# Kernel optimization log

Measured on AMD Instinct MI355X. Metric: run time of the kernel, lower is better.

Reference implementation:

```python
import jax, jax.numpy as jnp
import numpy as np

N_CAM = 6
N_HEADS = 8
N_POINTS = 4
D = 256  # internal d_model of the deformable attention


def _sine_pos(h, w, d=D):
    # DETR PositionEmbeddingSine, normalize=True, channels-last (h, w, d)
    npf = d // 2
    two_pi = 2.0 * np.pi
    y = jnp.arange(1, h + 1, dtype=jnp.float32) / (h + 1e-6) * two_pi
    x = jnp.arange(1, w + 1, dtype=jnp.float32) / (w + 1e-6) * two_pi
    dim_t = (10000.0 ** (2.0 * (jnp.arange(npf) // 2) / npf)).astype(jnp.float32)
    def enc(v):
        p = v[:, None] / dim_t
        return jnp.stack([jnp.sin(p[:, 0::2]), jnp.cos(p[:, 1::2])], axis=-1).reshape(v.shape[0], -1)
    py, px = enc(y), enc(x)
    return jnp.concatenate([
        jnp.broadcast_to(py[:, None, :], (h, w, npf)),
        jnp.broadcast_to(px[None, :, :], (h, w, npf))], axis=-1)


def _layernorm(x, g, b, eps=1e-5):
    mu = jnp.mean(x, -1, keepdims=True)
    var = jnp.mean((x - mu) ** 2, -1, keepdims=True)
    return (x - mu) * jax.lax.rsqrt(var + eps) * g + b


def _bilinear_gather(kv, loc_x, loc_y, H, W):
    # kv: (b, L, heads, H*W, c); loc_*: (b, Lq, heads, L, P) normalized to [0,1]
    # emulates F.grid_sample(mode='bilinear', padding_mode='zeros', align_corners=False)
    b, L, heads, HW, c = kv.shape
    _, Lq, _, _, P = loc_x.shape
    x = loc_x * W - 0.5
    y = loc_y * H - 0.5
    x0 = jnp.floor(x)
    y0 = jnp.floor(y)
    fx = x - x0
    fy = y - y0
    out = jnp.zeros((b, Lq, heads, L, P, c), kv.dtype)
    for dx in (0, 1):
        for dy in (0, 1):
            xi = x0 + dx
            yi = y0 + dy
            valid = (xi >= 0) & (xi < W) & (yi >= 0) & (yi < H)
            wgt = (fx if dx else 1.0 - fx) * (fy if dy else 1.0 - fy) * valid
            idx = (jnp.clip(yi, 0, H - 1) * W + jnp.clip(xi, 0, W - 1)).astype(jnp.int32)
            idx_t = idx.transpose(0, 3, 2, 1, 4).reshape(b, L, heads, Lq * P, 1)
            g = jnp.take_along_axis(kv, idx_t, axis=3)
            g = g.reshape(b, L, heads, Lq, P, c).transpose(0, 3, 2, 1, 4, 5)
            out = out + wgt[..., None] * g
    return out  # (b, Lq, heads, L, P, c)


def reference(x, conv0_w, conv0_b, conv2_w, conv2_b, cam_emb,
              off_w, off_b, val_w, val_b, key_w, key_b, out_w, out_b,
              conv1_w, conv1_b, norm0_g, norm0_b,
              lin1_w, lin1_b, lin2_w, lin2_b, norm2_g, norm2_b):
    bn, dim, H, W = x.shape
    b = bn // N_CAM
    hd = D // N_HEADS
    HW = H * W
    Lq = N_CAM * HW

    x_nhwc = x.transpose(0, 2, 3, 1)                  # (bn, H, W, dim)
    residual = x_nhwc.reshape(b, Lq, dim)             # b (n h w) d

    src = (x_nhwc @ conv0_w.T + conv0_b).reshape(b, N_CAM, H, W, D)  # conv0 1x1

    pos = _sine_pos(H, W)                              # (H, W, 256)
    spc = src + pos[None, None] + cam_emb[None, :, None, None, :]
    # per-level global descriptor: mean over pixels of conv2(src+pos+cam)
    g = jnp.mean((spc @ conv2_w.T + conv2_b).reshape(b, N_CAM, HW, D), axis=2)  # (b, n, 256)

    src_flat = src.reshape(b, Lq, D)
    query = spc.reshape(b, Lq, D)                      # src + cam + pos (flattened)

    value = src_flat @ val_w.T + val_b
    keys = src_flat @ key_w.T + key_b

    # sampling locations: per-query reference point + learned offsets (normalized)
    offsets = (query @ off_w.T + off_b).reshape(b, Lq, N_HEADS, N_CAM, N_POINTS, 2)
    ry, rx = jnp.meshgrid(
        (jnp.arange(H, dtype=jnp.float32) + 0.5) / H,
        (jnp.arange(W, dtype=jnp.float32) + 0.5) / W, indexing='ij')
    ref = jnp.tile(jnp.stack([rx.ravel(), ry.ravel()], -1), (N_CAM, 1))  # (Lq, 2) as (x, y)
    loc = ref[None, :, None, None, None, :] + offsets / jnp.array([W, H], jnp.float32)

    # gather keys and values in a single bilinear pass (concat on channel)
    kv = jnp.concatenate([
        keys.reshape(b, N_CAM, HW, N_HEADS, hd),
        value.reshape(b, N_CAM, HW, N_HEADS, hd)], axis=-1).transpose(0, 1, 3, 2, 4)
    sampled = _bilinear_gather(kv, loc[..., 0], loc[..., 1], H, W)  # (b,Lq,heads,L,P,2hd)
    k_s, v_s = sampled[..., :hd], sampled[..., hd:]

    # append per-level global token as an extra key/value point per level
    g_h = g.reshape(b, 1, N_CAM, N_HEADS, hd).transpose(0, 1, 3, 2, 4)[:, :, :, :, None, :]
    g_h = jnp.broadcast_to(g_h, (b, Lq, N_HEADS, N_CAM, 1, hd))
    k_all = jnp.concatenate([k_s, g_h], axis=4)        # (b,Lq,heads,L,P+1,hd)
    v_all = jnp.concatenate([v_s, g_h], axis=4)

    # key-aware attention: softmax over all (level, point) sampled keys
    q_h = query.reshape(b, Lq, N_HEADS, hd)
    logits = jnp.einsum('bqhd,bqhlpd->bqhlp', q_h, k_all) / jnp.sqrt(jnp.float32(hd))
    attn = jax.nn.softmax(logits.reshape(b, Lq, N_HEADS, -1), axis=-1).reshape(logits.shape)
    attn_out = jnp.einsum('bqhlp,bqhlpd->bqhd', attn, v_all).reshape(b, Lq, D)
    attn_out = attn_out @ out_w.T + out_b

    out = attn_out @ conv1_w.T + conv1_b               # conv1 1x1 back to dim
    out = _layernorm(residual + out, norm0_g, norm0_b)
    ffn = jax.nn.relu(out @ lin1_w.T + lin1_b) @ lin2_w.T + lin2_b
    out = _layernorm(out + ffn, norm2_g, norm2_b)

    return out.reshape(b, N_CAM, H, W, dim).transpose(0, 1, 4, 2, 3).reshape(bn, dim, H, W)


def setup_inputs() -> dict:
    key = jax.random.key(0)
    ks = jax.random.split(key, 16)
    B, DIM, H, W = 1, 256, 20, 40

    def w(k, shape, s=0.02):
        return jax.random.normal(k, shape, jnp.float32) * s

    n_off = N_HEADS * N_CAM * N_POINTS * 2
    return {
        "x": jax.random.normal(ks[0], (B * N_CAM, DIM, H, W), jnp.float32),
        "conv0_w": w(ks[1], (D, DIM)), "conv0_b": jnp.zeros((D,), jnp.float32),
        "conv2_w": w(ks[2], (D, D)), "conv2_b": jnp.zeros((D,), jnp.float32),
        "cam_emb": jax.random.uniform(ks[3], (N_CAM, D), jnp.float32),
        "off_w": w(ks[4], (n_off, D)),
        "off_b": jax.random.normal(ks[5], (n_off,), jnp.float32) * 0.5,
        "val_w": w(ks[6], (D, D)), "val_b": jnp.zeros((D,), jnp.float32),
        "key_w": w(ks[7], (D, D)), "key_b": jnp.zeros((D,), jnp.float32),
        "out_w": w(ks[8], (D, D)), "out_b": jnp.zeros((D,), jnp.float32),
        "conv1_w": w(ks[9], (DIM, D)), "conv1_b": jnp.zeros((DIM,), jnp.float32),
        "norm0_g": jnp.ones((DIM,), jnp.float32), "norm0_b": jnp.zeros((DIM,), jnp.float32),
        "lin1_w": w(ks[10], (DIM, DIM)), "lin1_b": jnp.zeros((DIM,), jnp.float32),
        "lin2_w": w(ks[11], (DIM, DIM)), "lin2_b": jnp.zeros((DIM,), jnp.float32),
        "norm2_g": jnp.ones((DIM,), jnp.float32), "norm2_b": jnp.zeros((DIM,), jnp.float32),
    }
```

## Files before the change

kernel.cpp:

```cpp
#include <hip/hip_runtime.h>
#include <math.h>

typedef unsigned short u16;
typedef unsigned int u32;

#define NCAM 6
#define NHEADS 8
#define NPOINTS 4
#define DD 256
#define HH 20
#define WW 40
#define HWSZ 800
#define LQ 4800
#define HDIM 32

typedef __attribute__((ext_vector_type(8))) short bf16x8;
typedef __attribute__((ext_vector_type(4))) float f32x4;

__device__ __forceinline__ u16 f2b(float x) {
    union { float f; u32 u; } v;
    v.f = x;
    u32 r = (v.u + 0x7FFFu + ((v.u >> 16) & 1u)) >> 16;
    return (u16)r;
}
__device__ __forceinline__ float lo2f(u32 u) {
    union { u32 u; float f; } v; v.u = u << 16; return v.f;
}
__device__ __forceinline__ float hi2f(u32 u) {
    union { u32 u; float f; } v; v.u = u & 0xFFFF0000u; return v.f;
}
__device__ __forceinline__ float red16(float s) {
    s += __shfl_xor(s, 1);
    s += __shfl_xor(s, 2);
    s += __shfl_xor(s, 4);
    s += __shfl_xor(s, 8);
    return s;
}

#define P1_BLOCKS 4570
__global__ __launch_bounds__(256) void prep1(
    const float* __restrict__ x, const float* __restrict__ conv0_w,
    const float* __restrict__ conv0_b, const float* __restrict__ key_w,
    const float* __restrict__ key_b, const float* __restrict__ val_w,
    const float* __restrict__ val_b, const float* __restrict__ off_w,
    const float* __restrict__ off_b, const float* __restrict__ lin1_w,
    const float* __restrict__ lin2_w, const float* __restrict__ conv1_w,
    const float* __restrict__ conv1_b, const float* __restrict__ out_w,
    const float* __restrict__ out_b, const float* __restrict__ cam_emb,
    float* __restrict__ pos, u16* __restrict__ xtb, float* __restrict__ mu_x,
    u16* __restrict__ Wcat, float* __restrict__ bias_cat,
    u16* __restrict__ conv1b, u16* __restrict__ lin1b, u16* __restrict__ lin2b,
    u16* __restrict__ off_wb, u16* __restrict__ kvpackb,
    u16* __restrict__ conv0_wTb, u16* __restrict__ out_wTb,
    float* __restrict__ bcomb, float* __restrict__ camoff,
    float* __restrict__ posy, float* __restrict__ posx) {
    __shared__ float sbuf[1088];
    int b = blockIdx.x, t = threadIdx.x;
    if (b < 800) {
        int hw = b, d = t;
        int h = hw / WW, w = hw % WW;
        int j = (d & 127) >> 1;
        float dim = powf(10000.0f, (float)j * (1.0f / 64.0f));
        float v;
        if (d < 128) v = (float)(h + 1) / (20.0f + 1e-6f) * (2.0f * (float)M_PI);
        else         v = (float)(w + 1) / (40.0f + 1e-6f) * (2.0f * (float)M_PI);
        float p = v / dim;
        pos[hw * DD + d] = (d & 1) ? cosf(p) : sinf(p);
    } else if (b < 1184) {
        int row = (b - 800) * 4 + (t >> 6);
        int lane = t & 63;
        const float* base = x + (size_t)row * HWSZ;
        float s = 0.f;
        for (int i = lane; i < HWSZ; i += 64) s += base[i];
#pragma unroll
        for (int m = 1; m <= 32; m <<= 1) s += __shfl_xor(s, m);
        if (lane == 0) mu_x[row] = s * (1.0f / (float)HWSZ);
    } else if (b < 3104) {
        int i = (b - 1184) * 256 + t;
        if (i < 65536) {
            Wcat[i] = f2b(conv0_w[i]);
            if (i < 256) bias_cat[i] = conv0_b[i];
        } else if (i < 131072) {
            conv1b[i - 65536] = f2b(conv1_w[i - 65536]);
        } else if (i < 196608) {
            lin1b[i - 131072] = f2b(lin1_w[i - 131072]);
        } else if (i < 262144) {
            lin2b[i - 196608] = f2b(lin2_w[i - 196608]);
        } else if (i < 360448) {
            off_wb[i - 262144] = f2b(off_w[i - 262144]);
        } else {
            int j = i - 360448;
            int rj = j >> 8, k = j & 255;
            int head = rj >> 6, cpair = (rj >> 1) & 31, kv = rj & 1;
            kvpackb[j] = f2b((kv ? val_w : key_w)[(size_t)(head * 32 + cpair) * 256 + k]);
        }
    } else if (b < 3232) {
        int idx = b - 3104;
        int which = idx >> 6;
        int t2 = idx & 63;
        int k0 = (t2 >> 3) * 32, c0 = (t2 & 7) * 32;
        const float* src = which ? out_w : conv0_w;
        u16* dst = which ? out_wTb : conv0_wTb;
        float (*tile)[33] = (float(*)[33])sbuf;
        int lc = t & 31, lk4 = t >> 5;
#pragma unroll
        for (int i = 0; i < 4; ++i) {
            int lk = lk4 * 4 + i;
            tile[lk][lc] = src[(size_t)(k0 + lk) * 256 + c0 + lc];
        }
        __syncthreads();
        int lk2 = t & 31, lc4 = t >> 5;
#pragma unroll
        for (int i = 0; i < 4; ++i) {
            int lc2 = lc4 * 4 + i;
            dst[(size_t)(c0 + lc2) * 256 + k0 + lk2] = f2b(tile[lk2][lc2]);
        }
    } else if (b < 4432) {
        int idx = b - 3232;
        int cam = idx / 200, rem = idx % 200;
        int hw0 = (rem % 25) * 32, c0 = (rem / 25) * 32;
        float (*tile)[33] = (float(*)[33])sbuf;
        int lhw = t & 31, lc4 = t >> 5;
#pragma unroll
        for (int i = 0; i < 4; ++i) {
            int lc = lc4 * 4 + i;
            tile[lc][lhw] = x[((size_t)(cam * DD + c0 + lc)) * HWSZ + hw0 + lhw];
        }
        __syncthreads();
        int lc2 = t & 31, lhw4 = t >> 5;
#pragma unroll
        for (int i = 0; i < 4; ++i) {
            int lhw2 = lhw4 * 4 + i;
            xtb[((size_t)(cam * HWSZ + hw0 + lhw2)) * DD + c0 + lc2] =
                f2b(tile[lc2][lhw2]);
        }
    } else if (b < 4492) {
        int idx = b - 4432;
        int yside = (idx < 20);
        int coord = yside ? idx : idx - 20;
        if (t < 128) {
            int d = t, j = d >> 1;
            float dim = powf(10000.0f, (float)j * (1.0f / 64.0f));
            float v = yside
                ? (float)(coord + 1) / (20.0f + 1e-6f) * (2.0f * (float)M_PI)
                : (float)(coord + 1) / (40.0f + 1e-6f) * (2.0f * (float)M_PI);
            float p = v / dim;
            sbuf[d] = (d & 1) ? cosf(p) : sinf(p);
        }
        __syncthreads();
        int koff = yside ? 0 : 128;
        float* outp = yside ? (posy + coord * 384) : (posx + coord * 384);
        int l = t & 15, og = t >> 4;
#pragma unroll
        for (int chunk = 0; chunk < 24; ++chunk) {
            int n = chunk * 16 + og;
            const float* wr = off_w + (size_t)n * 256 + koff + l * 8;
            float4 w0 = *(const float4*)wr;
            float4 w1 = *(const float4*)(wr + 4);
            const float* pv = sbuf + l * 8;
            float s = pv[0] * w0.x + pv[1] * w0.y + pv[2] * w0.z + pv[3] * w0.w +
                      pv[4] * w1.x + pv[5] * w1.y + pv[6] * w1.z + pv[7] * w1.w;
            s = red16(s);
            if (l == 0) outp[n] = s;
        }
    } else if (b < 4498) {
        int cam = b - 4492;
        sbuf[t] = cam_emb[cam * DD + t];
        __syncthreads();
        int l = t & 15, og = t >> 4;
#pragma unroll
        for (int chunk = 0; chunk < 24; ++chunk) {
            int n = chunk * 16 + og;
            const float* wr = off_w + (size_t)n * 256 + l * 16;
            float s = 0.f;
#pragma unroll
            for (int i = 0; i < 4; ++i) {
                float4 w4 = *(const float4*)(wr + i * 4);
                const float* ce = sbuf + l * 16 + i * 4;
                s += ce[0] * w4.x + ce[1] * w4.y + ce[2] * w4.z + ce[3] * w4.w;
            }
            s = red16(s);
            if (l == 0) camoff[cam * 384 + n] = s;
        }
    } else if (b < 4554) {
        sbuf[t] = conv0_b[t];
        __syncthreads();
        int l = t & 15, og = t >> 4;
        int rr = (b - 4498) * 16 + og;
        const float* srcp;
        float bsrc;
        if (rr < 512) {
            int head = rr >> 6, cpair = (rr >> 1) & 31, kv = rr & 1;
            srcp = (kv ? val_w : key_w) + (size_t)(head * 32 + cpair) * 256;
            bsrc = (kv ? val_b : key_b)[head * 32 + cpair];
        } else {
            srcp = off_w + (size_t)(rr - 512) * 256;
            bsrc = off_b[rr - 512];
        }
        float s = 0.f;
#pragma unroll
        for (int i = 0; i < 4; ++i) {
            float4 w4 = *(const float4*)(srcp + l * 16 + i * 4);
            const float* cb = sbuf + l * 16 + i * 4;
            s += cb[0] * w4.x + cb[1] * w4.y + cb[2] * w4.z + cb[3] * w4.w;
        }
        s = red16(s);
        if (l == 0) bias_cat[256 + rr] = bsrc + s;
    } else {
        sbuf[t] = out_b[t];
        __syncthreads();
        int l = t & 15, og = t >> 4;
        int n = (b - 4554) * 16 + og;
        float s = 0.f;
#pragma unroll
        for (int i = 0; i < 4; ++i) {
            float4 w4 = *(const float4*)(conv1_w + (size_t)n * 256 + l * 16 + i * 4);
            const float* ob = sbuf + l * 16 + i * 4;
            s += ob[0] * w4.x + ob[1] * w4.y + ob[2] * w4.z + ob[3] * w4.w;
        }
        s = red16(s);
        if (l == 0) bcomb[n] = conv1_b[n] + s;
    }
}

__global__ __launch_bounds__(256) void prep2(
    const u16* __restrict__ kvpackb, const u16* __restrict__ off_wb,
    const u16* __restrict__ conv0_wTb, const u16* __restrict__ conv1b,
    const u16* __restrict__ out_wTb, u16* __restrict__ Wcat,
    u16* __restrict__ wcombb) {
    __shared__ __align__(16) u16 As[1056];
    __shared__ __align__(16) u16 Bs[4120];
    int b = blockIdx.x, t = threadIdx.x;
    int isfold = (b < 56);
    int bb = isfold ? b : b - 56;
    int row0 = (bb >> 1) * 32, col0 = (bb & 1) * 128;
    const u16* Wb = isfold ? conv0_wTb : out_wTb;
    int wv = t >> 6, lane = t & 63;
    int quad = lane >> 4, l = lane & 15;
    f32x4 acc[2][2] = {};
    for (int k0 = 0; k0 < 256; k0 += 32) {
        __syncthreads();
        if (t < 128) {
            int m = t >> 2, j = t & 3;
            int rr = row0 + m;
            const u16* ap;
            if (isfold) ap = (rr < 512) ? (kvpackb + (size_t)rr * 256)
                                        : (off_wb + (size_t)(rr - 512) * 256);
            else        ap = conv1b + (size_t)rr * 256;
            *(uint4*)&As[(j * 33 + m) * 8] = *(const uint4*)&ap[k0 + j * 8];
        }
        {
            int n = t >> 1, jp = (t & 1) * 2;
            const u16* gsrc = &Wb[(size_t)(col0 + n) * 256 + k0 + jp * 8];
            *(uint4*)&Bs[(jp * 129 + n) * 8]       = *(const uint4*)gsrc;
            *(uint4*)&Bs[((jp + 1) * 129 + n) * 8] = *(const uint4*)(gsrc + 8);
        }
        __syncthreads();
        bf16x8 a0 = *(const bf16x8*)&As[(quad * 33 + l) * 8];
        bf16x8 a1 = *(const bf16x8*)&As[(quad * 33 + 16 + l) * 8];
        bf16x8 b0 = *(const bf16x8*)&Bs[(quad * 129 + wv * 32 + l) * 8];
        bf16x8 b1 = *(const bf16x8*)&Bs[(quad * 129 + wv * 32 + 16 + l) * 8];
        acc[0][0] = __builtin_amdgcn_mfma_f32_16x16x32_bf16(a0, b0, acc[0][0], 0, 0, 0);
        acc[0][1] = __builtin_amdgcn_mfma_f32_16x16x32_bf16(a0, b1, acc[0][1], 0, 0, 0);
        acc[1][0] = __builtin_amdgcn_mfma_f32_16x16x32_bf16(a1, b0, acc[1][0], 0, 0, 0);
        acc[1][1] = __builtin_amdgcn_mfma_f32_16x16x32_bf16(a1, b1, acc[1][1], 0, 0, 0);
    }
#pragma unroll
    for (int mt = 0; mt < 2; ++mt) {
#pragma unroll
        for (int nt = 0; nt < 2; ++nt) {
            int col = col0 + wv * 32 + nt * 16 + l;
#pragma unroll
            for (int r = 0; r < 4; ++r) {
                int rr = row0 + mt * 16 + quad * 4 + r;
                u16 ov = f2b(acc[mt][nt][r]);
                if (isfold) Wcat[(size_t)(256 + rr) * 256 + col] = ov;
                else        wcombb[(size_t)rr * 256 + col] = ov;
            }
        }
    }
}

__global__ __launch_bounds__(256) void gemm_fused(
    const u16* __restrict__ Ab, const u16* __restrict__ Wcat,
    const float* __restrict__ bias_cat, const float* __restrict__ pos,
    const float* __restrict__ cam_emb, u16* __restrict__ spcb,
    u16* __restrict__ kvcat16, float* __restrict__ offs,
    const float* __restrict__ mu_x, const float* __restrict__ conv0_w,
    const float* __restrict__ conv0_b, const float* __restrict__ conv2_w,
    const float* __restrict__ conv2_b, float* __restrict__ g) {
    int b = blockIdx.x, t = threadIdx.x;
    if (b < 675) {
        __shared__ __align__(16) u16 As[2080];
        __shared__ __align__(16) u16 Bs[4120];
        int col0 = (b % 9) * 128, row0 = (b / 9) * 64;
        int wv = t >> 6, lane = t & 63;
        int quad = lane >> 4, l = lane & 15;
        f32x4 acc[4][2] = {};
        for (int k0 = 0; k0 < 256; k0 += 32) {
            __syncthreads();
            {
                int m = t >> 2, j = t & 3;
                *(uint4*)&As[(j * 65 + m) * 8] =
                    *(const uint4*)&Ab[(size_t)(row0 + m) * 256 + k0 + j * 8];
            }
            {
                int n = t >> 1, jp = (t & 1) * 2;
                const u16* gsrc = &Wcat[(size_t)(col0 + n) * 256 + k0 + jp * 8];
                *(uint4*)&Bs[(jp * 129 + n) * 8]       = *(const uint4*)gsrc;
                *(uint4*)&Bs[((jp + 1) * 129 + n) * 8] = *(const uint4*)(gsrc + 8);
            }
            __syncthreads();
            bf16x8 b0 = *(const bf16x8*)&Bs[(quad * 129 + wv * 32 + l) * 8];
            bf16x8 b1 = *(const bf16x8*)&Bs[(quad * 129 + wv * 32 + 16 + l) * 8];
#pragma unroll
            for (int mt = 0; mt < 4; ++mt) {
                bf16x8 a = *(const bf16x8*)&As[(quad * 65 + mt * 16 + l) * 8];
                acc[mt][0] = __builtin_amdgcn_mfma_f32_16x16x32_bf16(a, b0, acc[mt][0], 0, 0, 0);
                acc[mt][1] = __builtin_amdgcn_mfma_f32_16x16x32_bf16(a, b1, acc[mt][1], 0, 0, 0);
            }
        }
#pragma unroll
        for (int mt = 0; mt < 4; ++mt) {
#pragma unroll
            for (int nt = 0; nt < 2; ++nt) {
                int col = col0 + wv * 32 + nt * 16 + l;
                float bb = bias_cat[col];
#pragma unroll
                for (int r = 0; r < 4; ++r) {
                    int row = row0 + mt * 16 + quad * 4 + r;
                    float v = acc[mt][nt][r] + bb;
                    if (col0 < 256) {
                        int cam = row / HWSZ, hw = row % HWSZ;
                        spcb[(size_t)row * 256 + col] =
                            f2b(v + pos[(size_t)hw * 256 + col] + cam_emb[cam * 256 + col]);
                    } else if (col0 < 768) {
                        kvcat16[(size_t)row * 512 + (col - 256)] = f2b(v);
                    } else {
                        offs[(size_t)row * 384 + (col - 768)] = v;
                    }
                }
            }
        }
    } else {
        int cam = b - 675;
        __shared__ float mu[DD];
        __shared__ float smu[DD];
        float pm;
        {
            int d = t;
            int j = (d & 127) >> 1;
            float inv = 1.0f / powf(10000.0f, (float)j * (1.0f / 64.0f));
            float s = 0.f;
            if (d < 128) {
                for (int h = 0; h < HH; ++h) {
                    float p = (float)(h + 1) / (20.0f + 1e-6f) * (2.0f * (float)M_PI) * inv;
                    s += (d & 1) ? cosf(p) : sinf(p);
                }
                pm = s * (1.0f / (float)HH);
            } else {
                for (int w = 0; w < WW; ++w) {
                    float p = (float)(w + 1) / (40.0f + 1e-6f) * (2.0f * (float)M_PI) * inv;
                    s += (d & 1) ? cosf(p) : sinf(p);
                }
                pm = s * (1.0f / (float)WW);
            }
        }
        mu[t] = mu_x[cam * DD + t];
        __syncthreads();
        float a = conv0_b[t] + pm + cam_emb[cam * DD + t];
        const float* wr = conv0_w + (size_t)t * DD;
        for (int k = 0; k < DD; ++k) a += mu[k] * wr[k];
        smu[t] = a;
        __syncthreads();
        float ga = conv2_b[t];
        const float* w2r = conv2_w + (size_t)t * DD;
        for (int d = 0; d < DD; ++d) ga += smu[d] * w2r[d];
        g[cam * DD + t] = ga;
    }
}

__global__ __launch_bounds__(256, 4) void attn_kernel(
    const u16* __restrict__ spcb, const u16* __restrict__ kvcat16,
    const float* __restrict__ offs, const float* __restrict__ posy,
    const float* __restrict__ posx, const float* __restrict__ camoff,
    const float* __restrict__ g, u16* __restrict__ attn_out) {
    int qq = blockIdx.x;
    int q0 = qq * 2;
    int tid = threadIdx.x;
    int cam = q0 / HWSZ;
    int hw0 = q0 % HWSZ;
    __shared__ float soff[2][384];
    __shared__ float wgt[2][192][4];
    __shared__ int   idxp[2][192][4];
    for (int i = tid; i < 768; i += 256) {
        int qi = i / 384, n = i - qi * 384;
        int hw = hw0 + qi;
        int h = hw / WW, w = hw - h * WW;
        soff[qi][n] = offs[(size_t)(q0 + qi) * 384 + n] + posy[h * 384 + n] +
                      posx[w * 384 + n] + camoff[cam * 384 + n];
    }
    __syncthreads();
    for (int e2 = tid; e2 < 384; e2 += 256) {
        int qi = e2 / 192, e = e2 - qi * 192;
        int head = e / 24, r = e - head * 24;
        int scam = r >> 2;
        int hw = hw0 + qi;
        int h = hw / WW, w = hw - h * WW;
        float X = (float)w + soff[qi][e * 2];
        float Y = (float)h + soff[qi][e * 2 + 1];
        float x0f = floorf(X), y0f = floorf(Y);
        float fx = X - x0f, fy = Y - y0f;
        int x0 = (int)x0f, y0 = (int)y0f, x1 = x0 + 1, y1 = y0 + 1;
        float vx0 = (x0 >= 0 && x0 < WW) ? 1.f : 0.f;
        float vx1 = (x1 >= 0 && x1 < WW) ? 1.f : 0.f;
        float vy0 = (y0 >= 0 && y0 < HH) ? 1.f : 0.f;
        float vy1 = (y1 >= 0 && y1 < HH) ? 1.f : 0.f;
        int cx0 = min(max(x0, 0), WW - 1), cx1 = min(max(x1, 0), WW - 1);
        int cy0 = min(max(y0, 0), HH - 1), cy1 = min(max(y1, 0), HH - 1);
        wgt[qi][e][0] = (1.f - fx) * (1.f - fy) * vx0 * vy0;
        wgt[qi][e][1] = fx * (1.f - fy) * vx1 * vy0;
        wgt[qi][e][2] = (1.f - fx) * fy * vx0 * vy1;
        wgt[qi][e][3] = fx * fy * vx1 * vy1;
        int pb = scam * HWSZ, hb = head * 64;
        idxp[qi][e][0] = ((pb + cy0 * WW + cx0) << 9) + hb;
        idxp[qi][e][1] = ((pb + cy0 * WW + cx1) << 9) + hb;
        idxp[qi][e][2] = ((pb + cy1 * WW + cx0) << 9) + hb;
        idxp[qi][e][3] = ((pb + cy1 * WW + cx1) << 9) + hb;
    }
    __syncthreads();
    int qi = tid >> 7, head = (tid >> 4) & 7, l = tid & 15;
    int q = q0 + qi;
    int c0 = l * 2;
    u32 qu = *(const u32*)&spcb[(size_t)q * 256 + head * 32 + c0];
    const float scale = 0.17677669529663687f;
    float q0s = lo2f(qu) * scale, q1s = hi2f(qu) * scale;
    float m = -1e30f, den = 0.f, o0 = 0.f, o1 = 0.f;
    int l4 = 4 * l;
    for (int scp = 0; scp < 3; ++scp) {
        int e0i = head * 24 + scp * 8;
        float av0[8], av1[8], lg[8];
#pragma unroll
        for (int p = 0; p < 8; ++p) {
            int e = e0i + p;
            float ak0 = 0.f, ak1 = 0.f, a0 = 0.f, a1 = 0.f;
#pragma unroll
            for (int j = 0; j < 4; ++j) {
                float wj = wgt[qi][e][j];
                int idx = idxp[qi][e][j] + l4;
                uint2 d = *(const uint2*)&kvcat16[idx];
                ak0 += wj * lo2f(d.x);
                a0  += wj * hi2f(d.x);
                ak1 += wj * lo2f(d.y);
                a1  += wj * hi2f(d.y);
            }
            av0[p] = a0; av1[p] = a1;
            float pl = q0s * ak0 + q1s * ak1;
            lg[p] = red16(pl);
        }
        float2 gva = *(const float2*)&g[(scp * 2) * 256 + head * 32 + c0];
        float2 gvb = *(const float2*)&g[(scp * 2 + 1) * 256 + head * 32 + c0];
        float pga = red16(q0s * gva.x + q1s * gva.y);
        float pgb = red16(q0s * gvb.x + q1s * gvb.y);
        float mc = fmaxf(pga, pgb);
#pragma unroll
        for (int p = 0; p < 8; ++p) mc = fmaxf(mc, lg[p]);
        float mn = fmaxf(m, mc);
        float aa = __expf(m - mn);
        float ee[8];
        float dsum = 0.f, s0 = 0.f, s1 = 0.f;
#pragma unroll
        for (int p = 0; p < 8; ++p) {
            ee[p] = __expf(lg[p] - mn);
            dsum += ee[p];
            s0 += ee[p] * av0[p];
            s1 += ee[p] * av1[p];
        }
        float ea = __expf(pga - mn), eb = __expf(pgb - mn);
        dsum += ea + eb;
        s0 += ea * gva.x + eb * gvb.x;
        s1 += ea * gva.y + eb * gvb.y;
        den = den * aa + dsum;
        o0 = o0 * aa + s0;
        o1 = o1 * aa + s1;
        m = mn;
    }
    float inv = 1.f / den;
    u32 pack = (u32)f2b(o0 * inv) | ((u32)f2b(o1 * inv) << 16);
    *(u32*)&attn_out[(size_t)q * 256 + head * 32 + c0] = pack;
}

__global__ __launch_bounds__(256) void epilogue(
    const u16* __restrict__ Ab, const u16* __restrict__ Wc,
    const float* __restrict__ bcomb, const float* __restrict__ x_nchw,
    const float* __restrict__ n0g, const float* __restrict__ n0b,
    const u16* __restrict__ W1, const float* __restrict__ b1v,
    const u16* __restrict__ W2, const float* __restrict__ b2v,
    const float* __restrict__ n2g, const float* __restrict__ n2b,
    float* __restrict__ out_nchw) {
    __shared__ __align__(16) u16 As[552];
    __shared__ __align__(16) u16 Bs[8232];
    __shared__ __align__(16) u16 A2[4360];
    __shared__ float red[4][4][4][2];
    int t = threadIdx.x;
    int row0 = blockIdx.x * 16;
    int wv = t >> 6, lane = t & 63, quad = lane >> 4, l = lane & 15;
    int cam = row0 / HWSZ;
    int hw0q = row0 % HWSZ + quad * 4;

    f32x4 acc[4] = {};
    for (int k0 = 0; k0 < 256; k0 += 32) {
        __syncthreads();
        if (t < 64) {
            int mm = t >> 2, j = t & 3;
            *(uint4*)&As[(j * 17 + mm) * 8] =
                *(const uint4*)&Ab[(size_t)(row0 + mm) * 256 + k0 + j * 8];
        }
#pragma unroll
        for (int j = 0; j < 4; ++j)
            *(uint4*)&Bs[(j * 257 + t) * 8] =
                *(const uint4*)&Wc[(size_t)t * 256 + k0 + j * 8];
        __syncthreads();
        bf16x8 a = *(const bf16x8*)&As[(quad * 17 + l) * 8];
#pragma unroll
        for (int nt = 0; nt < 4; ++nt) {
            bf16x8 b = *(const bf16x8*)&Bs[(quad * 257 + wv * 64 + nt * 16 + l) * 8];
            acc[nt] = __builtin_amdgcn_mfma_f32_16x16x32_bf16(a, b, acc[nt], 0, 0, 0);
        }
    }
    float v[4][4];
    int cols[4];
#pragma unroll
    for (int nt = 0; nt < 4; ++nt) {
        int col = wv * 64 + nt * 16 + l;
        cols[nt] = col;
        float bb = bcomb[col];
        float4 rx = *(const float4*)&x_nchw[((size_t)(cam * 256 + col)) * HWSZ + hw0q];
        v[nt][0] = acc[nt][0] + bb + rx.x;
        v[nt][1] = acc[nt][1] + bb + rx.y;
        v[nt][2] = acc[nt][2] + bb + rx.z;
        v[nt][3] = acc[nt][3] + bb + rx.w;
    }
#pragma unroll
    for (int r = 0; r < 4; ++r) {
        float s = v[0][r] + v[1][r] + v[2][r] + v[3][r];
        float sq = v[0][r] * v[0][r] + v[1][r] * v[1][r] +
                   v[2][r] * v[2][r] + v[3][r] * v[3][r];
#pragma unroll
        for (int msk = 1; msk <= 8; msk <<= 1) {
            s += __shfl_xor(s, msk);
            sq += __shfl_xor(sq, msk);
        }
        if (l == 0) { red[wv][quad][r][0] = s; red[wv][quad][r][1] = sq; }
    }
    __syncthreads();
    float o0[4][4];
#pragma unroll
    for (int r = 0; r < 4; ++r) {
        float S = red[0][quad][r][0] + red[1][quad][r][0] +
                  red[2][quad][r][0] + red[3][quad][r][0];
        float Q = red[0][quad][r][1] + red[1][quad][r][1] +
                  red[2][quad][r][1] + red[3][quad][r][1];
        float mean = S * (1.0f / 256.0f);
        float var = Q * (1.0f / 256.0f) - mean * mean;
        float rstd = rsqrtf(var + 1e-5f);
        int row = quad * 4 + r;
#pragma unroll
        for (int nt = 0; nt < 4; ++nt) {
            int col = cols[nt];
            float ov = (v[nt][r] - mean) * rstd * n0g[col] + n0b[col];
            o0[nt][r] = ov;
            A2[((col >> 3) * 17 + row) * 8 + (col & 7)] = f2b(ov);
        }
    }
    f32x4 acc2[4] = {};
    for (int k0 = 0; k0 < 256; k0 += 32) {
        __syncthreads();
#pragma unroll
        for (int j = 0; j < 4; ++j)
            *(uint4*)&Bs[(j * 257 + t) * 8] =
                *(const uint4*)&W1[(size_t)t * 256 + k0 + j * 8];
        __syncthreads();
        bf16x8 a = *(const bf16x8*)&A2[(((k0 >> 3) + quad) * 17 + l) * 8];
#pragma unroll
        for (int nt = 0; nt < 4; ++nt) {
            bf16x8 b = *(const bf16x8*)&Bs[(quad * 257 + wv * 64 + nt * 16 + l) * 8];
            acc2[nt] = __builtin_amdgcn_mfma_f32_16x16x32_bf16(a, b, acc2[nt], 0, 0, 0);
        }
    }
    __syncthreads();
#pragma unroll
    for (int nt = 0; nt < 4; ++nt) {
        int col = cols[nt];
        float bb = b1v[col];
#pragma unroll
        for (int r = 0; r < 4; ++r) {
            int row = quad * 4 + r;
            A2[((col >> 3) * 17 + row) * 8 + (col & 7)] = f2b(fmaxf(acc2[nt][r] + bb, 0.f));
        }
    }
    f32x4 acc3[4] = {};
    for (int k0 = 0; k0 < 256; k0 += 32) {
        __syncthreads();
#pragma unroll
        for (int j = 0; j < 4; ++j)
            *(uint4*)&Bs[(j * 257 + t) * 8] =
                *(const uint4*)&W2[(size_t)t * 256 + k0 + j * 8];
        __syncthreads();
        bf16x8 a = *(const bf16x8*)&A2[(((k0 >> 3) + quad) * 17 + l) * 8];
#pragma unroll
        for (int nt = 0; nt < 4; ++nt) {
            bf16x8 b = *(const bf16x8*)&Bs[(quad * 257 + wv * 64 + nt * 16 + l) * 8];
            acc3[nt] = __builtin_amdgcn_mfma_f32_16x16x32_bf16(a, b, acc3[nt], 0, 0, 0);
        }
    }
    float v2[4][4];
#pragma unroll
    for (int nt = 0; nt < 4; ++nt) {
        float bb = b2v[cols[nt]];
#pragma unroll
        for (int r = 0; r < 4; ++r) v2[nt][r] = acc3[nt][r] + bb + o0[nt][r];
    }
    __syncthreads();
#pragma unroll
    for (int r = 0; r < 4; ++r) {
        float s = v2[0][r] + v2[1][r] + v2[2][r] + v2[3][r];
        float sq = v2[0][r] * v2[0][r] + v2[1][r] * v2[1][r] +
                   v2[2][r] * v2[2][r] + v2[3][r] * v2[3][r];
#pragma unroll
        for (int msk = 1; msk <= 8; msk <<= 1) {
            s += __shfl_xor(s, msk);
            sq += __shfl_xor(sq, msk);
        }
        if (l == 0) { red[wv][quad][r][0] = s; red[wv][quad][r][1] = sq; }
    }
    __syncthreads();
    float mean2[4], rstd2[4];
#pragma unroll
    for (int r = 0; r < 4; ++r) {
        float S = red[0][quad][r][0] + red[1][quad][r][0] +
                  red[2][quad][r][0] + red[3][quad][r][0];
        float Q = red[0][quad][r][1] + red[1][quad][r][1] +
                  red[2][quad][r][1] + red[3][quad][r][1];
        mean2[r] = S * (1.0f / 256.0f);
        float var = Q * (1.0f / 256.0f) - mean2[r] * mean2[r];
        rstd2[r] = rsqrtf(var + 1e-5f);
    }
#pragma unroll
    for (int nt = 0; nt < 4; ++nt) {
        int col = cols[nt];
        float gg = n2g[col], bb = n2b[col];
        float4 ov4;
        ov4.x = (v2[nt][0] - mean2[0]) * rstd2[0] * gg + bb;
        ov4.y = (v2[nt][1] - mean2[1]) * rstd2[1] * gg + bb;
        ov4.z = (v2[nt][2] - mean2[2]) * rstd2[2] * gg + bb;
        ov4.w = (v2[nt][3] - mean2[3]) * rstd2[3] * gg + bb;
        *(float4*)&out_nchw[((size_t)(cam * 256 + col)) * HWSZ + hw0q] = ov4;
    }
}

extern "C" void kernel_launch(void* const* d_in, const int* in_sizes, int n_in,
                              void* d_out, int out_size, void* d_ws, size_t ws_size,
                              hipStream_t stream) {
    const float* x       = (const float*)d_in[0];
    const float* conv0_w = (const float*)d_in[1];
    const float* conv0_b = (const float*)d_in[2];
    const float* conv2_w = (const float*)d_in[3];
    const float* conv2_b = (const float*)d_in[4];
    const float* cam_emb = (const float*)d_in[5];
    const float* off_w   = (const float*)d_in[6];
    const float* off_b   = (const float*)d_in[7];
    const float* val_w   = (const float*)d_in[8];
    const float* val_b   = (const float*)d_in[9];
    const float* key_w   = (const float*)d_in[10];
    const float* key_b   = (const float*)d_in[11];
    const float* out_w   = (const float*)d_in[12];
    const float* out_b   = (const float*)d_in[13];
    const float* conv1_w = (const float*)d_in[14];
    const float* conv1_b = (const float*)d_in[15];
    const float* norm0_g = (const float*)d_in[16];
    const float* norm0_b = (const float*)d_in[17];
    const float* lin1_w  = (const float*)d_in[18];
    const float* lin1_b  = (const float*)d_in[19];
    const float* lin2_w  = (const float*)d_in[20];
    const float* lin2_b  = (const float*)d_in[21];
    const float* norm2_g = (const float*)d_in[22];
    const float* norm2_b = (const float*)d_in[23];

    float* ws = (float*)d_ws;
    const size_t SZ = (size_t)LQ * DD;
    float* pos      = ws;
    float* mu_x     = pos + 204800;
    float* g        = mu_x + 1536;
    float* camoff   = g + 1536;
    float* posy     = camoff + 2304;
    float* posx     = posy + 7680;
    float* bias_cat = posx + 15360;
    float* bcomb    = bias_cat + 1152;
    float* offs     = bcomb + 256;
    float* f_xtb    = offs + 1843200;
    float* f_spcb   = f_xtb + 614400;
    float* f_kvcat  = f_spcb + 614400;
    float* f_Wcat   = f_kvcat + 1228800;
    float* f_lin1b  = f_Wcat + 147456;
    float* f_lin2b  = f_lin1b + 32768;
    float* f_wcombb = f_lin2b + 32768;
    float* f_conv1b = f_wcombb + 32768;
    float* f_off_wb = f_conv1b + 32768;
    float* f_kvpack = f_off_wb + 49152;
    float* f_c0T    = f_kvpack + 65536;
    float* f_outT   = f_c0T + 32768;

    u16* xtb      = (u16*)f_xtb;
    u16* spcb     = (u16*)f_spcb;
    u16* kvcat16  = (u16*)f_kvcat;
    u16* Wcat     = (u16*)f_Wcat;
    u16* lin1b    = (u16*)f_lin1b;
    u16* lin2b    = (u16*)f_lin2b;
    u16* wcombb   = (u16*)f_wcombb;
    u16* conv1b   = (u16*)f_conv1b;
    u16* off_wb   = (u16*)f_off_wb;
    u16* kvpackb  = (u16*)f_kvpack;
    u16* conv0_wTb= (u16*)f_c0T;
    u16* out_wTb  = (u16*)f_outT;
    u16* attn_ob  = xtb;

    prep1<<<P1_BLOCKS, 256, 0, stream>>>(
        x, conv0_w, conv0_b, key_w, key_b, val_w, val_b, off_w, off_b,
        lin1_w, lin2_w, conv1_w, conv1_b, out_w, out_b, cam_emb,
        pos, xtb, mu_x, Wcat, bias_cat, conv1b, lin1b, lin2b,
        off_wb, kvpackb, conv0_wTb, out_wTb, bcomb, camoff, posy, posx);
    prep2<<<72, 256, 0, stream>>>(kvpackb, off_wb, conv0_wTb, conv1b, out_wTb,
                                  Wcat, wcombb);
    gemm_fused<<<681, 256, 0, stream>>>(xtb, Wcat, bias_cat, pos, cam_emb,
                                        spcb, kvcat16, offs, mu_x, conv0_w,
                                        conv0_b, conv2_w, conv2_b, g);
    attn_kernel<<<LQ / 2, 256, 0, stream>>>(spcb, kvcat16, offs, posy, posx,
                                            camoff, g, attn_ob);
    epilogue<<<300, 256, 0, stream>>>(attn_ob, wcombb, bcomb, x,
                                      norm0_g, norm0_b, lin1b, lin1_b,
                                      lin2b, lin2_b, norm2_g, norm2_b,
                                      (float*)d_out);
}
```

Before: 215.4 us.

## Pre-pack GEMM operands in k-group layout, load via global_load_lds, merge prep kernels

Activations and weights are now written in a k-major packed layout (groups of 8 bf16 along K, contiguous rows). This lets gemm_fused and the epilogue GEMMs stage tiles straight into LDS with global_load_lds instead of register round-trips. The weight-folding GEMMs from prep2 move into the single prep kernel, which reads fp32 weights and converts them inline, dropping one launch and several intermediate bf16 buffers. In exchange, LDS padding is removed, which may bring back bank conflicts, and the fold blocks run within a larger mixed-role grid.

```diff
diff --git a/kernel.cpp b/kernel.cpp
--- a/kernel.cpp
+++ b/kernel.cpp
@@ -36,9 +36,15 @@
     s += __shfl_xor(s, 8);
     return s;
 }
-
-#define P1_BLOCKS 4570
-__global__ __launch_bounds__(256) void prep1(
+__device__ __forceinline__ void gl_lds16(const void* g, void* l) {
+    __builtin_amdgcn_global_load_lds(
+        (const __attribute__((address_space(1))) void*)g,
+        (__attribute__((address_space(3))) void*)l, 16, 0, 0);
+}
+
+
+#define P1_BLOCKS 3362
+__global__ __launch_bounds__(256) void prep(
     const float* __restrict__ x, const float* __restrict__ conv0_w,
     const float* __restrict__ conv0_b, const float* __restrict__ key_w,
     const float* __restrict__ key_b, const float* __restrict__ val_w,
@@ -47,14 +53,15 @@
     const float* __restrict__ lin2_w, const float* __restrict__ conv1_w,
     const float* __restrict__ conv1_b, const float* __restrict__ out_w,
     const float* __restrict__ out_b, const float* __restrict__ cam_emb,
-    float* __restrict__ pos, u16* __restrict__ xtb, float* __restrict__ mu_x,
-    u16* __restrict__ Wcat, float* __restrict__ bias_cat,
-    u16* __restrict__ conv1b, u16* __restrict__ lin1b, u16* __restrict__ lin2b,
-    u16* __restrict__ off_wb, u16* __restrict__ kvpackb,
-    u16* __restrict__ conv0_wTb, u16* __restrict__ out_wTb,
-    float* __restrict__ bcomb, float* __restrict__ camoff,
-    float* __restrict__ posy, float* __restrict__ posx) {
+    float* __restrict__ pos, u16* __restrict__ xtb_t, float* __restrict__ mu_x,
+    u16* __restrict__ Wcat_t, float* __restrict__ bias_cat,
+    u16* __restrict__ lin1b_t, u16* __restrict__ lin2b_t,
+    u16* __restrict__ wcombb_t, float* __restrict__ bcomb,
+    float* __restrict__ camoff, float* __restrict__ posy,
+    float* __restrict__ posx) {
     __shared__ float sbuf[1088];
+    __shared__ __align__(16) u16 As2[1024];
+    __shared__ __align__(16) u16 Bs2[4096];
     int b = blockIdx.x, t = threadIdx.x;
     if (b < 800) {
         int hw = b, d = t;
@@ -75,48 +82,23 @@
 #pragma unroll
         for (int m = 1; m <= 32; m <<= 1) s += __shfl_xor(s, m);
         if (lane == 0) mu_x[row] = s * (1.0f / (float)HWSZ);
-    } else if (b < 3104) {
+    } else if (b < 1952) {
         int i = (b - 1184) * 256 + t;
         if (i < 65536) {
-            Wcat[i] = f2b(conv0_w[i]);
+            int n = i >> 8, k = i & 255;
+            Wcat_t[(((size_t)(k >> 3)) * 1152 + n) * 8 + (k & 7)] = f2b(conv0_w[i]);
             if (i < 256) bias_cat[i] = conv0_b[i];
         } else if (i < 131072) {
-            conv1b[i - 65536] = f2b(conv1_w[i - 65536]);
-        } else if (i < 196608) {
-            lin1b[i - 131072] = f2b(lin1_w[i - 131072]);
-        } else if (i < 262144) {
-            lin2b[i - 196608] = f2b(lin2_w[i - 196608]);
-        } else if (i < 360448) {
-            off_wb[i - 262144] = f2b(off_w[i - 262144]);
+            int j = i - 65536;
+            int n = j >> 8, k = j & 255;
+            lin1b_t[(((size_t)(k >> 3)) * 256 + n) * 8 + (k & 7)] = f2b(lin1_w[j]);
         } else {
-            int j = i - 360448;
-            int rj = j >> 8, k = j & 255;
-            int head = rj >> 6, cpair = (rj >> 1) & 31, kv = rj & 1;
-            kvpackb[j] = f2b((kv ? val_w : key_w)[(size_t)(head * 32 + cpair) * 256 + k]);
-        }
-    } else if (b < 3232) {
-        int idx = b - 3104;
-        int which = idx >> 6;
-        int t2 = idx & 63;
-        int k0 = (t2 >> 3) * 32, c0 = (t2 & 7) * 32;
-        const float* src = which ? out_w : conv0_w;
-        u16* dst = which ? out_wTb : conv0_wTb;
-        float (*tile)[33] = (float(*)[33])sbuf;
-        int lc = t & 31, lk4 = t >> 5;
-#pragma unroll
-        for (int i = 0; i < 4; ++i) {
-            int lk = lk4 * 4 + i;
-            tile[lk][lc] = src[(size_t)(k0 + lk) * 256 + c0 + lc];
-        }
-        __syncthreads();
-        int lk2 = t & 31, lc4 = t >> 5;
-#pragma unroll
-        for (int i = 0; i < 4; ++i) {
-            int lc2 = lc4 * 4 + i;
-            dst[(size_t)(c0 + lc2) * 256 + k0 + lk2] = f2b(tile[lk2][lc2]);
-        }
-    } else if (b < 4432) {
-        int idx = b - 3232;
+            int j = i - 131072;
+            int n = j >> 8, k = j & 255;
+            lin2b_t[(((size_t)(k >> 3)) * 256 + n) * 8 + (k & 7)] = f2b(lin2_w[j]);
+        }
+    } else if (b < 3152) {
+        int idx = b - 1952;
         int cam = idx / 200, rem = idx % 200;
         int hw0 = (rem % 25) * 32, c0 = (rem / 25) * 32;
         float (*tile)[33] = (float(*)[33])sbuf;
@@ -128,14 +110,16 @@
         }
         __syncthreads();
         int lc2 = t & 31, lhw4 = t >> 5;
+        int c = c0 + lc2;
 #pragma unroll
         for (int i = 0; i < 4; ++i) {
             int lhw2 = lhw4 * 4 + i;
-            xtb[((size_t)(cam * HWSZ + hw0 + lhw2)) * DD + c0 + lc2] =
+            int row = cam * HWSZ + hw0 + lhw2;
+            xtb_t[(((size_t)(c >> 3)) * 4800 + row) * 8 + (c & 7)] =
                 f2b(tile[lc2][lhw2]);
         }
-    } else if (b < 4492) {
-        int idx = b - 4432;
+    } else if (b < 3212) {
+        int idx = b - 3152;
         int yside = (idx < 20);
         int coord = yside ? idx : idx - 20;
         if (t < 128) {
@@ -163,8 +147,8 @@
             s = red16(s);
             if (l == 0) outp[n] = s;
         }
-    } else if (b < 4498) {
-        int cam = b - 4492;
+    } else if (b < 3218) {
+        int cam = b - 3212;
         sbuf[t] = cam_emb[cam * DD + t];
         __syncthreads();
         int l = t & 15, og = t >> 4;
@@ -182,11 +166,11 @@
             s = red16(s);
             if (l == 0) camoff[cam * 384 + n] = s;
         }
-    } else if (b < 4554) {
+    } else if (b < 3274) {
         sbuf[t] = conv0_b[t];
         __syncthreads();
         int l = t & 15, og = t >> 4;
-        int rr = (b - 4498) * 16 + og;
+        int rr = (b - 3218) * 16 + og;
         const float* srcp;
         float bsrc;
         if (rr < 512) {
@@ -206,11 +190,11 @@
         }
         s = red16(s);
         if (l == 0) bias_cat[256 + rr] = bsrc + s;
-    } else {
+    } else if (b < 3290) {
         sbuf[t] = out_b[t];
         __syncthreads();
         int l = t & 15, og = t >> 4;
-        int n = (b - 4554) * 16 + og;
+        int n = (b - 3274) * 16 + og;
         float s = 0.f;
 #pragma unroll
         for (int i = 0; i < 4; ++i) {
@@ -220,69 +204,84 @@
         }
         s = red16(s);
         if (l == 0) bcomb[n] = conv1_b[n] + s;
-    }
-}
-
-__global__ __launch_bounds__(256) void prep2(
-    const u16* __restrict__ kvpackb, const u16* __restrict__ off_wb,
-    const u16* __restrict__ conv0_wTb, const u16* __restrict__ conv1b,
-    const u16* __restrict__ out_wTb, u16* __restrict__ Wcat,
-    u16* __restrict__ wcombb) {
-    __shared__ __align__(16) u16 As[1056];
-    __shared__ __align__(16) u16 Bs[4120];
-    int b = blockIdx.x, t = threadIdx.x;
-    int isfold = (b < 56);
-    int bb = isfold ? b : b - 56;
-    int row0 = (bb >> 1) * 32, col0 = (bb & 1) * 128;
-    const u16* Wb = isfold ? conv0_wTb : out_wTb;
-    int wv = t >> 6, lane = t & 63;
-    int quad = lane >> 4, l = lane & 15;
-    f32x4 acc[2][2] = {};
-    for (int k0 = 0; k0 < 256; k0 += 32) {
-        __syncthreads();
-        if (t < 128) {
-            int m = t >> 2, j = t & 3;
-            int rr = row0 + m;
-            const u16* ap;
-            if (isfold) ap = (rr < 512) ? (kvpackb + (size_t)rr * 256)
-                                        : (off_wb + (size_t)(rr - 512) * 256);
-            else        ap = conv1b + (size_t)rr * 256;
-            *(uint4*)&As[(j * 33 + m) * 8] = *(const uint4*)&ap[k0 + j * 8];
-        }
-        {
-            int n = t >> 1, jp = (t & 1) * 2;
-            const u16* gsrc = &Wb[(size_t)(col0 + n) * 256 + k0 + jp * 8];
-            *(uint4*)&Bs[(jp * 129 + n) * 8]       = *(const uint4*)gsrc;
-            *(uint4*)&Bs[((jp + 1) * 129 + n) * 8] = *(const uint4*)(gsrc + 8);
-        }
-        __syncthreads();
-        bf16x8 a0 = *(const bf16x8*)&As[(quad * 33 + l) * 8];
-        bf16x8 a1 = *(const bf16x8*)&As[(quad * 33 + 16 + l) * 8];
-        bf16x8 b0 = *(const bf16x8*)&Bs[(quad * 129 + wv * 32 + l) * 8];
-        bf16x8 b1 = *(const bf16x8*)&Bs[(quad * 129 + wv * 32 + 16 + l) * 8];
-        acc[0][0] = __builtin_amdgcn_mfma_f32_16x16x32_bf16(a0, b0, acc[0][0], 0, 0, 0);
-        acc[0][1] = __builtin_amdgcn_mfma_f32_16x16x32_bf16(a0, b1, acc[0][1], 0, 0, 0);
-        acc[1][0] = __builtin_amdgcn_mfma_f32_16x16x32_bf16(a1, b0, acc[1][0], 0, 0, 0);
-        acc[1][1] = __builtin_amdgcn_mfma_f32_16x16x32_bf16(a1, b1, acc[1][1], 0, 0, 0);
-    }
-#pragma unroll
-    for (int mt = 0; mt < 2; ++mt) {
-#pragma unroll
-        for (int nt = 0; nt < 2; ++nt) {
-            int col = col0 + wv * 32 + nt * 16 + l;
-#pragma unroll
-            for (int r = 0; r < 4; ++r) {
-                int rr = row0 + mt * 16 + quad * 4 + r;
-                u16 ov = f2b(acc[mt][nt][r]);
-                if (isfold) Wcat[(size_t)(256 + rr) * 256 + col] = ov;
-                else        wcombb[(size_t)rr * 256 + col] = ov;
+    } else {
+        int fb = b - 3290;
+        int isw = (fb >= 56);
+        int bb = isw ? fb - 56 : fb;
+        int row0 = (bb >> 1) * 32, col0 = (bb & 1) * 128;
+        int wv = t >> 6, lane = t & 63, quad = lane >> 4, l = lane & 15;
+        f32x4 acc[2][2] = {};
+        for (int k0 = 0; k0 < 256; k0 += 32) {
+            __syncthreads();
+            if (t < 128) {
+                int m = t >> 2, j = t & 3;
+                int rr = row0 + m;
+                const float* ap;
+                if (!isw) {
+                    if (rr < 512) {
+                        int head = rr >> 6, cpair = (rr >> 1) & 31, kv = rr & 1;
+                        ap = (kv ? val_w : key_w) + (size_t)(head * 32 + cpair) * 256;
+                    } else {
+                        ap = off_w + (size_t)(rr - 512) * 256;
+                    }
+                } else {
+                    ap = conv1_w + (size_t)rr * 256;
+                }
+                float4 f0 = *(const float4*)&ap[k0 + j * 8];
+                float4 f1 = *(const float4*)&ap[k0 + j * 8 + 4];
+                uint4 up;
+                up.x = (u32)f2b(f0.x) | ((u32)f2b(f0.y) << 16);
+                up.y = (u32)f2b(f0.z) | ((u32)f2b(f0.w) << 16);
+                up.z = (u32)f2b(f1.x) | ((u32)f2b(f1.y) << 16);
+                up.w = (u32)f2b(f1.z) | ((u32)f2b(f1.w) << 16);
+                *(uint4*)&As2[(j * 32 + m) * 8] = up;
             }
+            {
+                int krel = t >> 3;
+                int k = k0 + krel;
+                int j = t >> 6, kin = k & 7;
+                int c0l = (t & 7) * 16;
+                const float* wsrc = (isw ? out_w : conv0_w) + (size_t)k * 256 + col0 + c0l;
+#pragma unroll
+                for (int i = 0; i < 16; i += 4) {
+                    float4 f = *(const float4*)&wsrc[i];
+                    Bs2[(j * 128 + c0l + i) * 8 + kin]     = f2b(f.x);
+                    Bs2[(j * 128 + c0l + i + 1) * 8 + kin] = f2b(f.y);
+                    Bs2[(j * 128 + c0l + i + 2) * 8 + kin] = f2b(f.z);
+                    Bs2[(j * 128 + c0l + i + 3) * 8 + kin] = f2b(f.w);
+                }
+            }
+            __syncthreads();
+            bf16x8 a0 = *(const bf16x8*)&As2[(quad * 32 + l) * 8];
+            bf16x8 a1 = *(const bf16x8*)&As2[(quad * 32 + 16 + l) * 8];
+            bf16x8 b0v = *(const bf16x8*)&Bs2[(quad * 128 + wv * 32 + l) * 8];
+            bf16x8 b1v = *(const bf16x8*)&Bs2[(quad * 128 + wv * 32 + 16 + l) * 8];
+            acc[0][0] = __builtin_amdgcn_mfma_f32_16x16x32_bf16(a0, b0v, acc[0][0], 0, 0, 0);
+            acc[0][1] = __builtin_amdgcn_mfma_f32_16x16x32_bf16(a0, b1v, acc[0][1], 0, 0, 0);
+            acc[1][0] = __builtin_amdgcn_mfma_f32_16x16x32_bf16(a1, b0v, acc[1][0], 0, 0, 0);
+            acc[1][1] = __builtin_amdgcn_mfma_f32_16x16x32_bf16(a1, b1v, acc[1][1], 0, 0, 0);
+        }
+#pragma unroll
+        for (int mt = 0; mt < 2; ++mt) {
+#pragma unroll
+            for (int nt = 0; nt < 2; ++nt) {
+                int c = col0 + wv * 32 + nt * 16 + l;
+#pragma unroll
+                for (int r = 0; r < 4; ++r) {
+                    int rr = row0 + mt * 16 + quad * 4 + r;
+                    u16 ov = f2b(acc[mt][nt][r]);
+                    if (!isw)
+                        Wcat_t[(((size_t)(c >> 3)) * 1152 + 256 + rr) * 8 + (c & 7)] = ov;
+                    else
+                        wcombb_t[(((size_t)(c >> 3)) * 256 + rr) * 8 + (c & 7)] = ov;
+                }
+            }
         }
     }
 }
 
 __global__ __launch_bounds__(256) void gemm_fused(
-    const u16* __restrict__ Ab, const u16* __restrict__ Wcat,
+    const u16* __restrict__ Abt, const u16* __restrict__ Wcat_t,
     const float* __restrict__ bias_cat, const float* __restrict__ pos,
     const float* __restrict__ cam_emb, u16* __restrict__ spcb,
     u16* __restrict__ kvcat16, float* __restrict__ offs,
@@ -291,31 +290,27 @@
     const float* __restrict__ conv2_b, float* __restrict__ g) {
     int b = blockIdx.x, t = threadIdx.x;
     if (b < 675) {
-        __shared__ __align__(16) u16 As[2080];
-        __shared__ __align__(16) u16 Bs[4120];
+        __shared__ __align__(16) u16 As[2048];
+        __shared__ __align__(16) u16 Bs[4096];
         int col0 = (b % 9) * 128, row0 = (b / 9) * 64;
         int wv = t >> 6, lane = t & 63;
         int quad = lane >> 4, l = lane & 15;
         f32x4 acc[4][2] = {};
-        for (int k0 = 0; k0 < 256; k0 += 32) {
+        for (int kg = 0; kg < 32; kg += 4) {
             __syncthreads();
-            {
-                int m = t >> 2, j = t & 3;
-                *(uint4*)&As[(j * 65 + m) * 8] =
-                    *(const uint4*)&Ab[(size_t)(row0 + m) * 256 + k0 + j * 8];
-            }
-            {
-                int n = t >> 1, jp = (t & 1) * 2;
-                const u16* gsrc = &Wcat[(size_t)(col0 + n) * 256 + k0 + jp * 8];
-                *(uint4*)&Bs[(jp * 129 + n) * 8]       = *(const uint4*)gsrc;
-                *(uint4*)&Bs[((jp + 1) * 129 + n) * 8] = *(const uint4*)(gsrc + 8);
-            }
+            gl_lds16(Abt + (((size_t)(kg + wv)) * 4800 + row0 + lane) * 8,
+                     &As[wv * 64 * 8]);
+            int jb = wv >> 1, hb = wv & 1;
+            gl_lds16(Wcat_t + (((size_t)(kg + jb)) * 1152 + col0 + hb * 64 + lane) * 8,
+                     &Bs[(jb * 128 + hb * 64) * 8]);
+            gl_lds16(Wcat_t + (((size_t)(kg + 2 + jb)) * 1152 + col0 + hb * 64 + lane) * 8,
+                     &Bs[((2 + jb) * 128 + hb * 64) * 8]);
             __syncthreads();
-            bf16x8 b0 = *(const bf16x8*)&Bs[(quad * 129 + wv * 32 + l) * 8];
-            bf16x8 b1 = *(const bf16x8*)&Bs[(quad * 129 + wv * 32 + 16 + l) * 8];
+            bf16x8 b0 = *(const bf16x8*)&Bs[(quad * 128 + wv * 32 + l) * 8];
+            bf16x8 b1 = *(const bf16x8*)&Bs[(quad * 128 + wv * 32 + 16 + l) * 8];
 #pragma unroll
             for (int mt = 0; mt < 4; ++mt) {
-                bf16x8 a = *(const bf16x8*)&As[(quad * 65 + mt * 16 + l) * 8];
+                bf16x8 a = *(const bf16x8*)&As[(quad * 64 + mt * 16 + l) * 8];
                 acc[mt][0] = __builtin_amdgcn_mfma_f32_16x16x32_bf16(a, b0, acc[mt][0], 0, 0, 0);
                 acc[mt][1] = __builtin_amdgcn_mfma_f32_16x16x32_bf16(a, b1, acc[mt][1], 0, 0, 0);
             }
@@ -491,15 +486,15 @@
 }
 
 __global__ __launch_bounds__(256) void epilogue(
-    const u16* __restrict__ Ab, const u16* __restrict__ Wc,
+    const u16* __restrict__ Ab, const u16* __restrict__ Wc_t,
     const float* __restrict__ bcomb, const float* __restrict__ x_nchw,
     const float* __restrict__ n0g, const float* __restrict__ n0b,
-    const u16* __restrict__ W1, const float* __restrict__ b1v,
-    const u16* __restrict__ W2, const float* __restrict__ b2v,
+    const u16* __restrict__ W1_t, const float* __restrict__ b1v,
+    const u16* __restrict__ W2_t, const float* __restrict__ b2v,
     const float* __restrict__ n2g, const float* __restrict__ n2b,
     float* __restrict__ out_nchw) {
     __shared__ __align__(16) u16 As[552];
-    __shared__ __align__(16) u16 Bs[8232];
+    __shared__ __align__(16) u16 Bs[8192];
     __shared__ __align__(16) u16 A2[4360];
     __shared__ float red[4][4][4][2];
     int t = threadIdx.x;
@@ -509,22 +504,22 @@
     int hw0q = row0 % HWSZ + quad * 4;
 
     f32x4 acc[4] = {};
-    for (int k0 = 0; k0 < 256; k0 += 32) {
+    for (int kg = 0; kg < 32; kg += 4) {
         __syncthreads();
         if (t < 64) {
             int mm = t >> 2, j = t & 3;
             *(uint4*)&As[(j * 17 + mm) * 8] =
-                *(const uint4*)&Ab[(size_t)(row0 + mm) * 256 + k0 + j * 8];
-        }
-#pragma unroll
-        for (int j = 0; j < 4; ++j)
-            *(uint4*)&Bs[(j * 257 + t) * 8] =
-                *(const uint4*)&Wc[(size_t)t * 256 + k0 + j * 8];
+                *(const uint4*)&Ab[(size_t)(row0 + mm) * 256 + kg * 8 + j * 8];
+        }
+#pragma unroll
+        for (int s = 0; s < 4; ++s)
+            gl_lds16(Wc_t + (((size_t)(kg + wv)) * 256 + s * 64 + lane) * 8,
+                     &Bs[(wv * 256 + s * 64) * 8]);
         __syncthreads();
         bf16x8 a = *(const bf16x8*)&As[(quad * 17 + l) * 8];
 #pragma unroll
         for (int nt = 0; nt < 4; ++nt) {
-            bf16x8 b = *(const bf16x8*)&Bs[(quad * 257 + wv * 64 + nt * 16 + l) * 8];
+            bf16x8 b = *(const bf16x8*)&Bs[(quad * 256 + wv * 64 + nt * 16 + l) * 8];
             acc[nt] = __builtin_amdgcn_mfma_f32_16x16x32_bf16(a, b, acc[nt], 0, 0, 0);
         }
     }
@@ -574,17 +569,17 @@
         }
     }
     f32x4 acc2[4] = {};
-    for (int k0 = 0; k0 < 256; k0 += 32) {
-        __syncthreads();
-#pragma unroll
-        for (int j = 0; j < 4; ++j)
-            *(uint4*)&Bs[(j * 257 + t) * 8] =
-                *(const uint4*)&W1[(size_t)t * 256 + k0 + j * 8];
-        __syncthreads();
-        bf16x8 a = *(const bf16x8*)&A2[(((k0 >> 3) + quad) * 17 + l) * 8];
+    for (int kg = 0; kg < 32; kg += 4) {
+        __syncthreads();
+#pragma unroll
+        for (int s = 0; s < 4; ++s)
+            gl_lds16(W1_t + (((size_t)(kg + wv)) * 256 + s * 64 + lane) * 8,
+                     &Bs[(wv * 256 + s * 64) * 8]);
+        __syncthreads();
+        bf16x8 a = *(const bf16x8*)&A2[((kg + quad) * 17 + l) * 8];
 #pragma unroll
         for (int nt = 0; nt < 4; ++nt) {
-            bf16x8 b = *(const bf16x8*)&Bs[(quad * 257 + wv * 64 + nt * 16 + l) * 8];
+            bf16x8 b = *(const bf16x8*)&Bs[(quad * 256 + wv * 64 + nt * 16 + l) * 8];
             acc2[nt] = __builtin_amdgcn_mfma_f32_16x16x32_bf16(a, b, acc2[nt], 0, 0, 0);
         }
     }
@@ -600,17 +595,17 @@
         }
     }
     f32x4 acc3[4] = {};
-    for (int k0 = 0; k0 < 256; k0 += 32) {
-        __syncthreads();
-#pragma unroll
-        for (int j = 0; j < 4; ++j)
-            *(uint4*)&Bs[(j * 257 + t) * 8] =
-                *(const uint4*)&W2[(size_t)t * 256 + k0 + j * 8];
-        __syncthreads();
-        bf16x8 a = *(const bf16x8*)&A2[(((k0 >> 3) + quad) * 17 + l) * 8];
+    for (int kg = 0; kg < 32; kg += 4) {
+        __syncthreads();
+#pragma unroll
+        for (int s = 0; s < 4; ++s)
+            gl_lds16(W2_t + (((size_t)(kg + wv)) * 256 + s * 64 + lane) * 8,
+                     &Bs[(wv * 256 + s * 64) * 8]);
+        __syncthreads();
+        bf16x8 a = *(const bf16x8*)&A2[((kg + quad) * 17 + l) * 8];
 #pragma unroll
         for (int nt = 0; nt < 4; ++nt) {
-            bf16x8 b = *(const bf16x8*)&Bs[(quad * 257 + wv * 64 + nt * 16 + l) * 8];
+            bf16x8 b = *(const bf16x8*)&Bs[(quad * 256 + wv * 64 + nt * 16 + l) * 8];
             acc3[nt] = __builtin_amdgcn_mfma_f32_16x16x32_bf16(a, b, acc3[nt], 0, 0, 0);
         }
     }
@@ -688,7 +683,6 @@
     const float* norm2_b = (const float*)d_in[23];
 
     float* ws = (float*)d_ws;
-    const size_t SZ = (size_t)LQ * DD;
     float* pos      = ws;
     float* mu_x     = pos + 204800;
     float* g        = mu_x + 1536;
@@ -705,40 +699,28 @@
     float* f_lin1b  = f_Wcat + 147456;
     float* f_lin2b  = f_lin1b + 32768;
     float* f_wcombb = f_lin2b + 32768;
-    float* f_conv1b = f_wcombb + 32768;
-    float* f_off_wb = f_conv1b + 32768;
-    float* f_kvpack = f_off_wb + 49152;
-    float* f_c0T    = f_kvpack + 65536;
-    float* f_outT   = f_c0T + 32768;
-
-    u16* xtb      = (u16*)f_xtb;
+
+    u16* xtb_t    = (u16*)f_xtb;
     u16* spcb     = (u16*)f_spcb;
     u16* kvcat16  = (u16*)f_kvcat;
-    u16* Wcat     = (u16*)f_Wcat;
-    u16* lin1b    = (u16*)f_lin1b;
-    u16* lin2b    = (u16*)f_lin2b;
-    u16* wcombb   = (u16*)f_wcombb;
-    u16* conv1b   = (u16*)f_conv1b;
-    u16* off_wb   = (u16*)f_off_wb;
-    u16* kvpackb  = (u16*)f_kvpack;
-    u16* conv0_wTb= (u16*)f_c0T;
-    u16* out_wTb  = (u16*)f_outT;
-    u16* attn_ob  = xtb;
-
-    prep1<<<P1_BLOCKS, 256, 0, stream>>>(
+    u16* Wcat_t   = (u16*)f_Wcat;
+    u16* lin1b_t  = (u16*)f_lin1b;
+    u16* lin2b_t  = (u16*)f_lin2b;
+    u16* wcombb_t = (u16*)f_wcombb;
+    u16* attn_ob  = xtb_t;
+
+    prep<<<P1_BLOCKS, 256, 0, stream>>>(
         x, conv0_w, conv0_b, key_w, key_b, val_w, val_b, off_w, off_b,
         lin1_w, lin2_w, conv1_w, conv1_b, out_w, out_b, cam_emb,
-        pos, xtb, mu_x, Wcat, bias_cat, conv1b, lin1b, lin2b,
-        off_wb, kvpackb, conv0_wTb, out_wTb, bcomb, camoff, posy, posx);
-    prep2<<<72, 256, 0, stream>>>(kvpackb, off_wb, conv0_wTb, conv1b, out_wTb,
-                                  Wcat, wcombb);
-    gemm_fused<<<681, 256, 0, stream>>>(xtb, Wcat, bias_cat, pos, cam_emb,
+        pos, xtb_t, mu_x, Wcat_t, bias_cat, lin1b_t, lin2b_t, wcombb_t,
+        bcomb, camoff, posy, posx);
+    gemm_fused<<<681, 256, 0, stream>>>(xtb_t, Wcat_t, bias_cat, pos, cam_emb,
                                         spcb, kvcat16, offs, mu_x, conv0_w,
                                         conv0_b, conv2_w, conv2_b, g);
     attn_kernel<<<LQ / 2, 256, 0, stream>>>(spcb, kvcat16, offs, posy, posx,
                                             camoff, g, attn_ob);
-    epilogue<<<300, 256, 0, stream>>>(attn_ob, wcombb, bcomb, x,
-                                      norm0_g, norm0_b, lin1b, lin1_b,
-                                      lin2b, lin2_b, norm2_g, norm2_b,
+    epilogue<<<300, 256, 0, stream>>>(attn_ob, wcombb_t, bcomb, x,
+                                      norm0_g, norm0_b, lin1b_t, lin1_b,
+                                      lin2b_t, lin2_b, norm2_g, norm2_b,
                                       (float*)d_out);
 }
```

Measured after the change: 200.8 us. 6.8% less time.
